# Optimization experiments

Hardware: AMD Instinct MI355X
Metric: run time of the kernel (lower is better)

The kernel has to match this reference:

```python
import jax, jax.numpy as jnp
import numpy as np

B, C, H, W = 8, 128, 256, 256
D = 64            # embed_dim
S = 32            # max_segments


def setup_inputs() -> dict:
    key = jax.random.key(0)
    ks = jax.random.split(key, 8)
    return {
        "segment_labels": jax.random.randint(ks[0], (B, 1, H, W), 0, S, dtype=jnp.int32),
        "features": jax.random.normal(ks[1], (B, C, H, W), jnp.float32),
        # 1x1 conv stack feat_proj: Conv2d(C->D), ReLU, Conv2d(D->D)
        "conv1_w": jax.random.normal(ks[2], (D, C), jnp.float32) * 0.05,
        "conv1_b": jnp.zeros((D,), jnp.float32),
        "conv2_w": jax.random.normal(ks[3], (D, D), jnp.float32) * 0.1,
        "conv2_b": jnp.zeros((D,), jnp.float32),
        # nn.Embedding(max_segments + 1, embed_dim)
        "embed_table": jax.random.normal(ks[4], (S + 1, D), jnp.float32) * 0.02,
        # nn.Linear(2*D, D): y = x @ W.T + b, W is (out, in)
        "out_w": jax.random.normal(ks[5], (D, 2 * D), jnp.float32) * 0.05,
        "out_b": jnp.zeros((D,), jnp.float32),
    }


def reference(segment_labels, features, conv1_w, conv1_b, conv2_w, conv2_b,
              embed_table, out_w, out_b):
    Bb, Cc, Hh, Ww = features.shape
    P = Hh * Ww
    Smax = embed_table.shape[0] - 1  # max_segments

    # feat_proj: two 1x1 convs == per-pixel GEMMs
    x = features.reshape(Bb, Cc, P)                                   # (B,C,P)
    h1 = jnp.maximum(jnp.einsum('oc,bcp->bpo', conv1_w, x) + conv1_b, 0.0)  # (B,P,D)
    feat = jnp.einsum('od,bpd->bpo', conv2_w, h1) + conv2_b           # (B,P,D)

    # Per-(batch, segment-id) masked mean via a single segment-sum pass.
    labels = segment_labels[:, 0].reshape(Bb, P)                       # (B,P) in [0,S)
    ids = (labels + Smax * jnp.arange(Bb, dtype=labels.dtype)[:, None]).reshape(-1)
    sums = jax.ops.segment_sum(feat.reshape(Bb * P, -1), ids,
                               num_segments=Bb * Smax).reshape(Bb, Smax, -1)
    counts = jax.ops.segment_sum(jnp.ones((Bb * P,), feat.dtype), ids,
                                 num_segments=Bb * Smax).reshape(Bb, Smax)
    pooled = sums / jnp.maximum(counts, 1.0)[..., None]                # (B,S,D) (zeros where absent)

    # type embedding for seg_id s (already in [0,S), clamp is a no-op but faithful)
    type_emb = embed_table[jnp.clip(jnp.arange(Smax), 0, Smax)]        # (S,D)
    combined = jnp.concatenate(
        [pooled, jnp.broadcast_to(type_emb, (Bb, Smax, type_emb.shape[-1]))], axis=-1)
    combined = jnp.einsum('oe,bse->bso', out_w, combined) + out_b      # (B,S,D)

    # torch.unique returns sorted present labels; compact present segments to the
    # front (rank order), pad rest with zeros.
    present = counts > 0                                               # (B,S)
    rank = jnp.cumsum(present.astype(jnp.int32), axis=1) - 1
    dst = jnp.where(present, rank, Smax)                               # Smax = dropped slot
    bidx = jnp.broadcast_to(jnp.arange(Bb)[:, None], (Bb, Smax))
    out = jnp.zeros_like(combined)
    out = out.at[bidx, dst].set(combined, mode='drop')
    return out
```

## Files before the change

kernel.cpp:

```cpp
#include <hip/hip_runtime.h>


#define B_ 8
#define C_ 128
#define P_ 65536
#define D_ 64
#define S_ 32
#define WPB 4
#define TMW 128
#define TMB (WPB * TMW)

typedef short  bf16x8 __attribute__((ext_vector_type(8)));
typedef float  f32x4  __attribute__((ext_vector_type(4)));

__device__ __forceinline__ short f2bf(float f) {
  union { float f; unsigned u; } v; v.f = f;
  unsigned r = v.u + 0x7fffu + ((v.u >> 16) & 1u);
  return (short)(r >> 16);
}

__global__ __launch_bounds__(256) void w1_to_bf16(const float* __restrict__ w1,
                                                  short* __restrict__ wbf) {
  int i = blockIdx.x * 256 + threadIdx.x;
  if (i < C_ * D_) wbf[i] = f2bf(w1[i]);
}

__global__ __launch_bounds__(256, 4) void proj_mfma(
    const int* __restrict__ labels, const float* __restrict__ feat,
    const short* __restrict__ wbf, const float* __restrict__ b1,
    float* __restrict__ gsum, int* __restrict__ gcnt)
{
  __shared__ __align__(16) char wlds[D_ * 256];
  __shared__ float s_acc[S_][68];
  __shared__ int   s_cnt[S_];

  const int tid  = threadIdx.x;
  const int wave = tid >> 6, l = tid & 63, m = l & 15, g = l >> 4;
  const int b    = blockIdx.y;
  const int px0  = blockIdx.x * TMB;

  #pragma unroll
  for (int i = 0; i < 4; ++i) {
    const int e = tid * 32 + i * 8;
    const int row = e >> 7, colB = (e & 127) * 2;
    *(bf16x8*)&wlds[row * 256 + (colB ^ ((row & 7) << 4))] =
        *(const bf16x8*)&wbf[e];
  }
  for (int i = tid; i < S_ * 68; i += 256) ((float*)s_acc)[i] = 0.f;
  if (tid < S_) s_cnt[tid] = 0;
  __syncthreads();

  const float* xpg = feat + (size_t)b * C_ * P_ + (size_t)(g * 8) * P_
                   + px0 + wave * TMW + m;
  const int*   lb  = labels + (size_t)b * P_ + px0 + wave * TMW;
  const int    xsw = (m & 7) << 4;

  float b1v[4];
  #pragma unroll
  for (int nt = 0; nt < 4; ++nt) b1v[nt] = b1[nt * 16 + m];

  float xvA[4][8], xvB[4][8];

#define ISSUE(dst, t_) do {                                                   \
    _Pragma("unroll") for (int kk = 0; kk < 4; ++kk)                          \
    _Pragma("unroll") for (int j = 0; j < 8; ++j)                             \
      dst[kk][j] = xpg[(size_t)(kk * 32 + j) * P_ + (t_) * 16];               \
  } while (0)

#define COMPUTE(src, t_) do {                                                 \
    f32x4 acc[4] = {{0,0,0,0},{0,0,0,0},{0,0,0,0},{0,0,0,0}};                 \
    _Pragma("unroll") for (int ks = 0; ks < 4; ++ks) {                        \
      bf16x8 af;                                                              \
      _Pragma("unroll") for (int j = 0; j < 8; ++j) af[j] = f2bf(src[ks][j]); \
      _Pragma("unroll") for (int nt = 0; nt < 4; ++nt) {                      \
        bf16x8 bwv = *(const bf16x8*)&wlds[(nt * 16 + m) * 256 +              \
                                           ((ks * 64 + g * 16) ^ xsw)];       \
        acc[nt] = __builtin_amdgcn_mfma_f32_16x16x32_bf16(af, bwv,            \
                                                          acc[nt], 0, 0, 0);  \
      }                                                                       \
    }                                                                         \
    const int4 lv = *(const int4*)&lb[(t_) * 16 + g * 4];                     \
    _Pragma("unroll") for (int nt = 0; nt < 4; ++nt)                          \
      _Pragma("unroll") for (int r = 0; r < 4; ++r) {                         \
        const int lab = ((r & 2) ? ((r & 1) ? lv.w : lv.z)                    \
                                 : ((r & 1) ? lv.y : lv.x)) & (S_ - 1);       \
        atomicAdd(&s_acc[lab][nt * 16 + m],                                   \
                  fmaxf(acc[nt][r] + b1v[nt], 0.f));                          \
      }                                                                       \
    if (m < 4) {                                                              \
      const int lab = ((m & 2) ? ((m & 1) ? lv.w : lv.z)                      \
                               : ((m & 1) ? lv.y : lv.x)) & (S_ - 1);         \
      atomicAdd(&s_cnt[lab], 1);                                              \
    }                                                                         \
  } while (0)

  ISSUE(xvA, 0);
  __builtin_amdgcn_sched_barrier(0);
  #pragma unroll
  for (int t = 0; t < 8; t += 2) {
    ISSUE(xvB, t + 1);
    __builtin_amdgcn_sched_barrier(0);
    COMPUTE(xvA, t);
    __builtin_amdgcn_sched_barrier(0);
    if (t + 2 < 8) {
      ISSUE(xvA, t + 2);
      __builtin_amdgcn_sched_barrier(0);
    }
    COMPUTE(xvB, t + 1);
    __builtin_amdgcn_sched_barrier(0);
  }
#undef ISSUE
#undef COMPUTE

  __syncthreads();
  for (int i = tid; i < S_ * D_; i += 256)
    atomicAdd(&gsum[(size_t)b * S_ * D_ + i], s_acc[i >> 6][i & 63]);
  if (tid < S_) atomicAdd(&gcnt[b * S_ + tid], s_cnt[tid]);
}

__global__ __launch_bounds__(64) void seg_finalize2(
    const float* __restrict__ gsum, const int* __restrict__ gcnt,
    const float* __restrict__ w2, const float* __restrict__ b2,
    const float* __restrict__ emb, const float* __restrict__ wo,
    const float* __restrict__ bo, float* __restrict__ out)
{
  const int s = blockIdx.x, b = blockIdx.y, o = threadIdx.x;
  const int co = (o < S_) ? gcnt[b * S_ + o] : 0;
  const unsigned long long mask = __ballot(co > 0);
  const int cnt = gcnt[b * S_ + s];
  if (cnt <= 0) return;
  const int rank = __popcll(mask & ((1ull << s) - 1ull));

  __shared__ float s_mean[D_], s_pool[D_];
  s_mean[o] = gsum[((size_t)b * S_ + s) * D_ + o] * (1.f / (float)cnt);
  __syncthreads();
  float pooled = b2[o];
  #pragma unroll
  for (int d = 0; d < D_; ++d) pooled += w2[o * D_ + d] * s_mean[d];
  s_pool[o] = pooled;
  __syncthreads();
  float r = bo[o];
  #pragma unroll
  for (int e = 0; e < D_; ++e) r += wo[o * 2 * D_ + e] * s_pool[e];
  #pragma unroll
  for (int e = 0; e < D_; ++e) r += wo[o * 2 * D_ + D_ + e] * emb[s * D_ + e];
  out[((size_t)b * S_ + rank) * D_ + o] = r;
}

extern "C" void kernel_launch(void* const* d_in, const int* in_sizes, int n_in,
                              void* d_out, int out_size, void* d_ws, size_t ws_size,
                              hipStream_t stream) {
  const int*   labels = (const int*)  d_in[0];
  const float* feat   = (const float*)d_in[1];
  const float* w1     = (const float*)d_in[2];
  const float* b1     = (const float*)d_in[3];
  const float* w2     = (const float*)d_in[4];
  const float* b2     = (const float*)d_in[5];
  const float* emb    = (const float*)d_in[6];
  const float* wo     = (const float*)d_in[7];
  const float* bo     = (const float*)d_in[8];
  float* out = (float*)d_out;

  char* w = (char*)d_ws;
  float* gsum = (float*)w;   w += (size_t)B_ * S_ * D_ * 4;
  int*   gcnt = (int*)w;     w += (size_t)B_ * S_ * 4;
  short* wbf  = (short*)w;

  hipMemsetAsync(d_ws, 0, (size_t)B_ * S_ * D_ * 4 + (size_t)B_ * S_ * 4, stream);
  hipMemsetAsync(d_out, 0, (size_t)out_size * sizeof(float), stream);

  w1_to_bf16<<<(C_ * D_ + 255) / 256, 256, 0, stream>>>(w1, wbf);

  dim3 grid(P_ / TMB, B_);
  proj_mfma<<<grid, 256, 0, stream>>>(labels, feat, wbf, b1, gsum, gcnt);
  seg_finalize2<<<dim3(S_, B_), 64, 0, stream>>>(gsum, gcnt, w2, b2, emb, wo, bo, out);
}
```

Measured before the change: 203.4 us.

## Stream feature tiles into LDS with async global_load_lds triple-buffered pipeline

Replaces register-based double-buffered global loads with asynchronous global_load_lds transfers into a per-wave 4-slot LDS ring. Loads are issued three stages ahead and gated by explicit vmcnt waits. The W1 bf16 fragments are now held in registers, loaded once from LDS, so the inner loop no longer reads weights from LDS. Each block covers twice as many pixels and labels are staged in LDS. The aim is to keep more memory traffic in flight and hide HBM latency. The cost is more LDS per block, lower occupancy (launch bounds 2) and reliance on hand-tuned wait counts.

```diff
diff --git a/kernel.cpp b/kernel.cpp
--- a/kernel.cpp
+++ b/kernel.cpp
@@ -7,11 +7,11 @@
 #define D_ 64
 #define S_ 32
 #define WPB 4
-#define TMW 128
-#define TMB (WPB * TMW)
-
-typedef short  bf16x8 __attribute__((ext_vector_type(8)));
-typedef float  f32x4  __attribute__((ext_vector_type(4)));
+#define PXW 256
+#define TMB (WPB * PXW)
+
+typedef short bf16x8 __attribute__((ext_vector_type(8)));
+typedef float f32x4  __attribute__((ext_vector_type(4)));
 
 __device__ __forceinline__ short f2bf(float f) {
   union { float f; unsigned u; } v; v.f = f;
@@ -25,61 +25,87 @@
   if (i < C_ * D_) wbf[i] = f2bf(w1[i]);
 }
 
-__global__ __launch_bounds__(256, 4) void proj_mfma(
+__device__ __forceinline__ void gload4(const float* g, const float* l) {
+  __builtin_amdgcn_global_load_lds(
+      (const __attribute__((address_space(1))) float*)g,
+      (__attribute__((address_space(3))) float*)l, 4, 0, 0);
+}
+
+__global__ __launch_bounds__(256, 2) void proj_mfma(
     const int* __restrict__ labels, const float* __restrict__ feat,
     const short* __restrict__ wbf, const float* __restrict__ b1,
     float* __restrict__ gsum, int* __restrict__ gcnt)
 {
-  __shared__ __align__(16) char wlds[D_ * 256];
+  __shared__ __align__(16) float xpipe[WPB][4][64 * 16];
+  __shared__ int   lab_lds[TMB];
   __shared__ float s_acc[S_][68];
   __shared__ int   s_cnt[S_];
+  __shared__ float s_b1[D_];
 
   const int tid  = threadIdx.x;
   const int wave = tid >> 6, l = tid & 63, m = l & 15, g = l >> 4;
   const int b    = blockIdx.y;
   const int px0  = blockIdx.x * TMB;
 
-  #pragma unroll
-  for (int i = 0; i < 4; ++i) {
-    const int e = tid * 32 + i * 8;
-    const int row = e >> 7, colB = (e & 127) * 2;
-    *(bf16x8*)&wlds[row * 256 + (colB ^ ((row & 7) << 4))] =
-        *(const bf16x8*)&wbf[e];
-  }
+  *(int4*)&lab_lds[tid * 4] = *(const int4*)&labels[(size_t)b * P_ + px0 + tid * 4];
   for (int i = tid; i < S_ * 68; i += 256) ((float*)s_acc)[i] = 0.f;
   if (tid < S_) s_cnt[tid] = 0;
-  __syncthreads();
-
-  const float* xpg = feat + (size_t)b * C_ * P_ + (size_t)(g * 8) * P_
-                   + px0 + wave * TMW + m;
-  const int*   lb  = labels + (size_t)b * P_ + px0 + wave * TMW;
-  const int    xsw = (m & 7) << 4;
-
+  if (tid < D_) s_b1[tid] = b1[tid];
+  {
+    short* wst = (short*)&xpipe[0][0][0];
+    for (int i = tid; i < C_ * D_ / 8; i += 256)
+      ((bf16x8*)wst)[i] = ((const bf16x8*)wbf)[i];
+  }
+  __syncthreads();
+  bf16x8 bfr[4][4];
+  #pragma unroll
+  for (int nt = 0; nt < 4; ++nt)
+    #pragma unroll
+    for (int ks = 0; ks < 4; ++ks)
+      bfr[nt][ks] = *(const bf16x8*)&((const short*)&xpipe[0][0][0])
+                        [(nt * 16 + m) * C_ + ks * 32 + g * 8];
   float b1v[4];
   #pragma unroll
-  for (int nt = 0; nt < 4; ++nt) b1v[nt] = b1[nt * 16 + m];
-
-  float xvA[4][8], xvB[4][8];
-
-#define ISSUE(dst, t_) do {                                                   \
-    _Pragma("unroll") for (int kk = 0; kk < 4; ++kk)                          \
-    _Pragma("unroll") for (int j = 0; j < 8; ++j)                             \
-      dst[kk][j] = xpg[(size_t)(kk * 32 + j) * P_ + (t_) * 16];               \
+  for (int nt = 0; nt < 4; ++nt) b1v[nt] = s_b1[nt * 16 + m];
+  __syncthreads();
+
+  const float* xg = feat + (size_t)b * C_ * P_ + (size_t)g * P_
+                  + px0 + wave * PXW + m;
+
+#define STAGE(c_) do {                                                        \
+    const int t_ = (c_) >> 1, h_ = (c_) & 1;                                  \
+    const float* gb_ = xg + (size_t)(h_ * 64) * P_ + t_ * 16;                 \
+    const float* lb_ = &xpipe[wave][(c_) & 3][0];                             \
+    _Pragma("unroll") for (int i = 0; i < 16; ++i)                            \
+      gload4(gb_ + (size_t)(i * 4) * P_, lb_ + i * 64);                       \
   } while (0)
 
-#define COMPUTE(src, t_) do {                                                 \
-    f32x4 acc[4] = {{0,0,0,0},{0,0,0,0},{0,0,0,0},{0,0,0,0}};                 \
-    _Pragma("unroll") for (int ks = 0; ks < 4; ++ks) {                        \
+#define WAITV(n_) asm volatile("s_waitcnt vmcnt(" #n_ ")" ::: "memory");      \
+                  __builtin_amdgcn_sched_barrier(0)
+
+#define CONSUME0(t_) do {                                                     \
+    const float* cb_ = &xpipe[wave][(2 * (t_)) & 3][0];                       \
+    _Pragma("unroll") for (int kk = 0; kk < 2; ++kk) {                        \
       bf16x8 af;                                                              \
-      _Pragma("unroll") for (int j = 0; j < 8; ++j) af[j] = f2bf(src[ks][j]); \
-      _Pragma("unroll") for (int nt = 0; nt < 4; ++nt) {                      \
-        bf16x8 bwv = *(const bf16x8*)&wlds[(nt * 16 + m) * 256 +              \
-                                           ((ks * 64 + g * 16) ^ xsw)];       \
-        acc[nt] = __builtin_amdgcn_mfma_f32_16x16x32_bf16(af, bwv,            \
-                                                          acc[nt], 0, 0, 0);  \
-      }                                                                       \
+      _Pragma("unroll") for (int j = 0; j < 8; ++j)                           \
+        af[j] = f2bf(cb_[(kk * 32 + g * 8 + j) * 16 + m]);                    \
+      _Pragma("unroll") for (int nt = 0; nt < 4; ++nt)                        \
+        acc[nt] = __builtin_amdgcn_mfma_f32_16x16x32_bf16(af, bfr[nt][kk],    \
+                                                          acc[nt], 0, 0, 0); \
     }                                                                         \
-    const int4 lv = *(const int4*)&lb[(t_) * 16 + g * 4];                     \
+  } while (0)
+
+#define CONSUME1(t_) do {                                                     \
+    const float* cb_ = &xpipe[wave][(2 * (t_) + 1) & 3][0];                   \
+    _Pragma("unroll") for (int kk = 0; kk < 2; ++kk) {                        \
+      bf16x8 af;                                                              \
+      _Pragma("unroll") for (int j = 0; j < 8; ++j)                           \
+        af[j] = f2bf(cb_[(kk * 32 + g * 8 + j) * 16 + m]);                    \
+      _Pragma("unroll") for (int nt = 0; nt < 4; ++nt)                        \
+        acc[nt] = __builtin_amdgcn_mfma_f32_16x16x32_bf16(af, bfr[nt][2 + kk],\
+                                                          acc[nt], 0, 0, 0); \
+    }                                                                         \
+    const int4 lv = *(const int4*)&lab_lds[wave * PXW + (t_) * 16 + g * 4];   \
     _Pragma("unroll") for (int nt = 0; nt < 4; ++nt)                          \
       _Pragma("unroll") for (int r = 0; r < 4; ++r) {                         \
         const int lab = ((r & 2) ? ((r & 1) ? lv.w : lv.z)                    \
@@ -94,23 +120,30 @@
     }                                                                         \
   } while (0)
 
-  ISSUE(xvA, 0);
-  __builtin_amdgcn_sched_barrier(0);
-  #pragma unroll
-  for (int t = 0; t < 8; t += 2) {
-    ISSUE(xvB, t + 1);
-    __builtin_amdgcn_sched_barrier(0);
-    COMPUTE(xvA, t);
-    __builtin_amdgcn_sched_barrier(0);
-    if (t + 2 < 8) {
-      ISSUE(xvA, t + 2);
-      __builtin_amdgcn_sched_barrier(0);
-    }
-    COMPUTE(xvB, t + 1);
-    __builtin_amdgcn_sched_barrier(0);
+  f32x4 acc[4];
+  STAGE(0); STAGE(1); STAGE(2);
+
+  for (int t2 = 0; t2 < 15; ++t2) {
+    WAITV(32);
+    STAGE(2 * t2 + 3);
+    #pragma unroll
+    for (int nt = 0; nt < 4; ++nt) acc[nt] = (f32x4){0.f, 0.f, 0.f, 0.f};
+    CONSUME0(t2);
+    WAITV(32);
+    if (t2 < 14) STAGE(2 * t2 + 4);
+    CONSUME1(t2);
   }
-#undef ISSUE
-#undef COMPUTE
+  WAITV(16);
+  #pragma unroll
+  for (int nt = 0; nt < 4; ++nt) acc[nt] = (f32x4){0.f, 0.f, 0.f, 0.f};
+  CONSUME0(15);
+  WAITV(0);
+  CONSUME1(15);
+
+#undef STAGE
+#undef WAITV
+#undef CONSUME0
+#undef CONSUME1
 
   __syncthreads();
   for (int i = tid; i < S_ * D_; i += 256)
```

After: 219.3 us. 7.8% more time.
